# Kernel optimization log

Measured on AMD Instinct MI355X. Metric: run time of the kernel, lower is better.

Reference implementation:

```python
import jax, jax.numpy as jnp
import numpy as np


def setup_inputs() -> dict:
    key = jax.random.key(0)
    kq, kk, kv = jax.random.split(key, 3)
    B, H, S, D = 2, 16, 2048, 128
    q = jax.random.normal(kq, (B, H, S, D), dtype=jnp.float32)
    k = jax.random.normal(kk, (B, H, S, D), dtype=jnp.float32)
    v = jax.random.normal(kv, (B, H, S, D), dtype=jnp.float32)
    return {"q": q, "k": k, "v": v}


def reference(q, k, v):
    # qk: [B,H,S,S] full score matrix (faithful to the naive torch module)
    qk = jnp.einsum("bhsd,bhtd->bhst", q, k)
    m = jnp.max(qk, axis=-1, keepdims=True)          # row max
    p = jnp.exp(qk - m)                               # unnormalized probs
    # NOTE: original module computes lse but returns only the UNNORMALIZED o.
    o = jnp.einsum("bhst,bhtd->bhsd", p, v)
    return o
```

## Files before the change

### kernel.cpp

```cpp
#include <hip/hip_runtime.h>

typedef _Float16 f16x8  __attribute__((ext_vector_type(8)));
typedef _Float16 f16x4  __attribute__((ext_vector_type(4)));
typedef _Float16 f16x2  __attribute__((ext_vector_type(2)));
typedef float    f32x4  __attribute__((ext_vector_type(4)));
typedef float    f32x16 __attribute__((ext_vector_type(16)));

#define MFMA32(a, b, c) __builtin_amdgcn_mfma_f32_32x32x16_f16((a), (b), (c), 0, 0, 0)

static constexpr int SEQ   = 2048;
static constexpr int DIM   = 128;
static constexpr int QBLK  = 128;
static constexpr int KVBLK = 32;
static constexpr int NKT   = SEQ / KVBLK;
static constexpr int BH    = 2 * 16;
static constexpr int KSTR  = 136;
static constexpr int VSTR  = 40;

__global__ __launch_bounds__(256, 2)
void fa_fwd_kernel(const float* __restrict__ Qg, const float* __restrict__ Kg,
                   const float* __restrict__ Vg, float* __restrict__ Og)
{
    __shared__ __align__(16) _Float16 Ksh[KVBLK * KSTR];
    __shared__ __align__(16) _Float16 Vt[DIM * VSTR];

    const int tid  = threadIdx.x;
    const int wv   = tid >> 6;
    const int lane = tid & 63;
    const int lq   = lane & 31;
    const int lh   = lane >> 5;

    const int bi = blockIdx.x;
    const int bh = (bi & 7) + 8 * (bi >> 7);
    const int qt = (bi >> 3) & 15;

    const size_t base = (size_t)bh * SEQ * DIM;
    const float* Qp = Qg + base;
    const float* Kp = Kg + base;
    const float* Vp = Vg + base;
    float*       Op = Og + base;

    const int q0 = qt * QBLK + wv * 32;

    constexpr float LOG2E = 1.44269504088896340736f;
    f16x8 qh[8];
    {
        const float* qs = Qp + (size_t)(q0 + lq) * DIM + 8 * lh;
#pragma unroll
        for (int t = 0; t < 8; ++t) {
            const float4 a = *(const float4*)(qs + 16 * t);
            const float4 b = *(const float4*)(qs + 16 * t + 4);
            float xs[8] = {a.x, a.y, a.z, a.w, b.x, b.y, b.z, b.w};
            f16x8 h;
#pragma unroll
            for (int e = 0; e < 8; ++e) h[e] = (_Float16)(xs[e] * LOG2E);
            qh[t] = h;
        }
    }

    f32x16 acc[4];
#pragma unroll
    for (int a = 0; a < 4; ++a)
#pragma unroll
        for (int r = 0; r < 16; ++r) acc[a][r] = 0.0f;

    float mrow  = -3.0e38f;
    float mtrue = -3.0e38f;

    const int ksr = tid >> 3, kc0 = (tid & 7) * 16;
    const int vc  = tid & 31;
    const int vk  = (tid >> 5) * 4;
    const float* kb = Kp + (size_t)ksr * DIM + kc0;
    const float* vb = Vp + (size_t)vk * DIM + vc;

    float4 kreg[4];
    float  vreg[4][4];
#pragma unroll
    for (int t = 0; t < 4; ++t) kreg[t] = *(const float4*)(kb + t * 4);
#pragma unroll
    for (int j = 0; j < 4; ++j)
#pragma unroll
        for (int r = 0; r < 4; ++r) vreg[j][r] = vb[(size_t)r * DIM + 32 * j];

    for (int kt = 0; kt < NKT; ++kt) {
        __syncthreads();

#pragma unroll
        for (int g = 0; g < 2; ++g) {
            float xs[8] = {kreg[2*g].x, kreg[2*g].y, kreg[2*g].z, kreg[2*g].w,
                           kreg[2*g+1].x, kreg[2*g+1].y, kreg[2*g+1].z, kreg[2*g+1].w};
            f16x8 h;
#pragma unroll
            for (int e = 0; e < 8; ++e) h[e] = (_Float16)xs[e];
            *(f16x8*)((char*)Ksh + (ksr * KSTR + kc0 + 8 * g) * 2) = h;
        }
#pragma unroll
        for (int j = 0; j < 4; ++j) {
            const int d = vc + 32 * j;
            f16x4 tv = {(_Float16)vreg[j][0], (_Float16)vreg[j][1],
                        (_Float16)vreg[j][2], (_Float16)vreg[j][3]};
            *(f16x4*)((char*)Vt + (d * VSTR + vk) * 2) = tv;
        }
        __syncthreads();

        if (kt + 1 < NKT) {
            const float* ks_ = kb + (size_t)(kt + 1) * KVBLK * DIM;
            const float* vs_ = vb + (size_t)(kt + 1) * KVBLK * DIM;
#pragma unroll
            for (int t = 0; t < 4; ++t) kreg[t] = *(const float4*)(ks_ + t * 4);
#pragma unroll
            for (int j = 0; j < 4; ++j)
#pragma unroll
                for (int r = 0; r < 4; ++r) vreg[j][r] = vs_[(size_t)r * DIM + 32 * j];
        }

        f32x16 s0, s1;
#pragma unroll
        for (int r = 0; r < 16; ++r) { s0[r] = 0.0f; s1[r] = 0.0f; }
        __builtin_amdgcn_s_setprio(1);
#pragma unroll
        for (int t = 0; t < 4; ++t) {
            f16x8 ka = *(const f16x8*)((const char*)Ksh + (lq * KSTR + 32 * t + 8 * lh) * 2);
            f16x8 kc = *(const f16x8*)((const char*)Ksh + (lq * KSTR + 32 * t + 16 + 8 * lh) * 2);
            s0 = MFMA32(ka, qh[2 * t], s0);
            s1 = MFMA32(kc, qh[2 * t + 1], s1);
        }
        __builtin_amdgcn_s_setprio(0);
        f32x16 st = s0 + s1;

        float tmax = fmaxf(fmaxf(fmaxf(st[0], st[1]), fmaxf(st[2], st[3])),
                           fmaxf(fmaxf(st[4], st[5]), fmaxf(st[6], st[7])));
        tmax = fmaxf(tmax, fmaxf(fmaxf(fmaxf(st[8], st[9]), fmaxf(st[10], st[11])),
                                 fmaxf(fmaxf(st[12], st[13]), fmaxf(st[14], st[15]))));
        tmax = fmaxf(tmax, __shfl_xor(tmax, 32));
        mtrue = fmaxf(mtrue, tmax);

        if (!__all(tmax - mrow <= 6.0f)) {
            const float mn  = fmaxf(mrow, tmax);
            const float scl = __builtin_exp2f(mrow - mn);
            mrow = mn;
#pragma unroll
            for (int a = 0; a < 4; ++a)
#pragma unroll
                for (int r = 0; r < 16; ++r) acc[a][r] *= scl;
        }

        int pk[8];
#pragma unroll
        for (int i = 0; i < 8; ++i) {
            f16x2 e = {(_Float16)__builtin_exp2f(st[2 * i] - mrow),
                       (_Float16)__builtin_exp2f(st[2 * i + 1] - mrow)};
            pk[i] = __builtin_bit_cast(int, e);
        }

#pragma unroll
        for (int s = 0; s < 2; ++s) {
            const int z1 = __shfl_xor(lh ? pk[4*s+0] : pk[4*s+2], 32);
            const int z2 = __shfl_xor(lh ? pk[4*s+1] : pk[4*s+3], 32);
            union { int i[4]; f16x8 v; } u;
            u.i[0] = lh ? z1 : pk[4*s+0];
            u.i[1] = lh ? z2 : pk[4*s+1];
            u.i[2] = lh ? pk[4*s+2] : z1;
            u.i[3] = lh ? pk[4*s+3] : z2;
            const f16x8 pb = u.v;
            __builtin_amdgcn_s_setprio(1);
#pragma unroll
            for (int dm = 0; dm < 4; ++dm) {
                const int d = dm * 32 + lq;
                f16x8 va = *(const f16x8*)((const char*)Vt + (d * VSTR + 16 * s + 8 * lh) * 2);
                acc[dm] = MFMA32(va, pb, acc[dm]);
            }
            __builtin_amdgcn_s_setprio(0);
        }
    }

    const float fin = __builtin_exp2f(mrow - mtrue);
#pragma unroll
    for (int a = 0; a < 4; ++a)
#pragma unroll
        for (int r = 0; r < 16; ++r) acc[a][r] *= fin;

    float* ob = Op + (size_t)(q0 + lq) * DIM + 4 * lh;
#pragma unroll
    for (int dm = 0; dm < 4; ++dm)
#pragma unroll
        for (int kp = 0; kp < 4; ++kp) {
            f32x4 v4 = {acc[dm][4*kp], acc[dm][4*kp+1], acc[dm][4*kp+2], acc[dm][4*kp+3]};
            *(f32x4*)(ob + dm * 32 + kp * 8) = v4;
        }
}

extern "C" void kernel_launch(void* const* d_in, const int* in_sizes, int n_in,
                              void* d_out, int out_size, void* d_ws, size_t ws_size,
                              hipStream_t stream) {
    const float* q = (const float*)d_in[0];
    const float* k = (const float*)d_in[1];
    const float* v = (const float*)d_in[2];
    float* o = (float*)d_out;
    dim3 grid((SEQ / QBLK) * BH);
    fa_fwd_kernel<<<grid, dim3(256), 0, stream>>>(q, k, v, o);
}
```

Before: 121.5 us.

## Double KV tile to 64 rows and convert K/V to fp16 before the barrier

Doubles the KV tile from 32 to 64 keys, halving the number of loop iterations and their barriers. QK^T now computes two independent 32-key score tiles over the full head dimension instead of splitting the head dimension and summing. The fp16 conversion of prefetched K/V is moved ahead of the first barrier so only the LDS stores sit between the barriers, and the lazy-rescale threshold is loosened from 6 to 10. The cost is roughly double the prefetch registers (K/V staging plus fp16 copies) under a launch bound of 2 blocks per CU, which risks spills or lower occupancy, and the looser threshold lets fp16 probabilities grow larger.

```diff
diff --git a/kernel.cpp b/kernel.cpp
--- a/kernel.cpp
+++ b/kernel.cpp
@@ -11,11 +11,11 @@
 static constexpr int SEQ   = 2048;
 static constexpr int DIM   = 128;
 static constexpr int QBLK  = 128;
-static constexpr int KVBLK = 32;
+static constexpr int KVBLK = 64;
 static constexpr int NKT   = SEQ / KVBLK;
 static constexpr int BH    = 2 * 16;
 static constexpr int KSTR  = 136;
-static constexpr int VSTR  = 40;
+static constexpr int VSTR  = 72;
 
 __global__ __launch_bounds__(256, 2)
 void fa_fwd_kernel(const float* __restrict__ Qg, const float* __restrict__ Kg,
@@ -67,39 +67,49 @@
     float mrow  = -3.0e38f;
     float mtrue = -3.0e38f;
 
-    const int ksr = tid >> 3, kc0 = (tid & 7) * 16;
+    const int ksr = tid >> 2, kc0 = (tid & 3) * 32;
     const int vc  = tid & 31;
-    const int vk  = (tid >> 5) * 4;
+    const int vk  = (tid >> 5) * 8;
     const float* kb = Kp + (size_t)ksr * DIM + kc0;
     const float* vb = Vp + (size_t)vk * DIM + vc;
 
-    float4 kreg[4];
-    float  vreg[4][4];
-#pragma unroll
-    for (int t = 0; t < 4; ++t) kreg[t] = *(const float4*)(kb + t * 4);
+    float4 kreg[8];
+    float  vreg[4][8];
+#pragma unroll
+    for (int t = 0; t < 8; ++t) kreg[t] = *(const float4*)(kb + t * 4);
 #pragma unroll
     for (int j = 0; j < 4; ++j)
 #pragma unroll
-        for (int r = 0; r < 4; ++r) vreg[j][r] = vb[(size_t)r * DIM + 32 * j];
+        for (int r = 0; r < 8; ++r) vreg[j][r] = vb[(size_t)r * DIM + 32 * j];
 
     for (int kt = 0; kt < NKT; ++kt) {
-        __syncthreads();
-
-#pragma unroll
-        for (int g = 0; g < 2; ++g) {
+        f16x8 kh16[4], vh16[4];
+#pragma unroll
+        for (int g = 0; g < 4; ++g) {
             float xs[8] = {kreg[2*g].x, kreg[2*g].y, kreg[2*g].z, kreg[2*g].w,
                            kreg[2*g+1].x, kreg[2*g+1].y, kreg[2*g+1].z, kreg[2*g+1].w};
             f16x8 h;
 #pragma unroll
             for (int e = 0; e < 8; ++e) h[e] = (_Float16)xs[e];
-            *(f16x8*)((char*)Ksh + (ksr * KSTR + kc0 + 8 * g) * 2) = h;
-        }
+            kh16[g] = h;
+        }
+#pragma unroll
+        for (int j = 0; j < 4; ++j) {
+            f16x8 h;
+#pragma unroll
+            for (int r = 0; r < 8; ++r) h[r] = (_Float16)vreg[j][r];
+            vh16[j] = h;
+        }
+
+        __syncthreads();
+
+#pragma unroll
+        for (int g = 0; g < 4; ++g)
+            *(f16x8*)((char*)Ksh + (ksr * KSTR + kc0 + 8 * g) * 2) = kh16[g];
 #pragma unroll
         for (int j = 0; j < 4; ++j) {
             const int d = vc + 32 * j;
-            f16x4 tv = {(_Float16)vreg[j][0], (_Float16)vreg[j][1],
-                        (_Float16)vreg[j][2], (_Float16)vreg[j][3]};
-            *(f16x4*)((char*)Vt + (d * VSTR + vk) * 2) = tv;
+            *(f16x8*)((char*)Vt + (d * VSTR + vk) * 2) = vh16[j];
         }
         __syncthreads();
 
@@ -107,11 +117,11 @@
             const float* ks_ = kb + (size_t)(kt + 1) * KVBLK * DIM;
             const float* vs_ = vb + (size_t)(kt + 1) * KVBLK * DIM;
 #pragma unroll
-            for (int t = 0; t < 4; ++t) kreg[t] = *(const float4*)(ks_ + t * 4);
+            for (int t = 0; t < 8; ++t) kreg[t] = *(const float4*)(ks_ + t * 4);
 #pragma unroll
             for (int j = 0; j < 4; ++j)
 #pragma unroll
-                for (int r = 0; r < 4; ++r) vreg[j][r] = vs_[(size_t)r * DIM + 32 * j];
+                for (int r = 0; r < 8; ++r) vreg[j][r] = vs_[(size_t)r * DIM + 32 * j];
         }
 
         f32x16 s0, s1;
@@ -119,23 +129,21 @@
         for (int r = 0; r < 16; ++r) { s0[r] = 0.0f; s1[r] = 0.0f; }
         __builtin_amdgcn_s_setprio(1);
 #pragma unroll
-        for (int t = 0; t < 4; ++t) {
-            f16x8 ka = *(const f16x8*)((const char*)Ksh + (lq * KSTR + 32 * t + 8 * lh) * 2);
-            f16x8 kc = *(const f16x8*)((const char*)Ksh + (lq * KSTR + 32 * t + 16 + 8 * lh) * 2);
-            s0 = MFMA32(ka, qh[2 * t], s0);
-            s1 = MFMA32(kc, qh[2 * t + 1], s1);
+        for (int t = 0; t < 8; ++t) {
+            f16x8 ka = *(const f16x8*)((const char*)Ksh + (lq * KSTR + 16 * t + 8 * lh) * 2);
+            f16x8 kc = *(const f16x8*)((const char*)Ksh + ((lq + 32) * KSTR + 16 * t + 8 * lh) * 2);
+            s0 = MFMA32(ka, qh[t], s0);
+            s1 = MFMA32(kc, qh[t], s1);
         }
         __builtin_amdgcn_s_setprio(0);
-        f32x16 st = s0 + s1;
-
-        float tmax = fmaxf(fmaxf(fmaxf(st[0], st[1]), fmaxf(st[2], st[3])),
-                           fmaxf(fmaxf(st[4], st[5]), fmaxf(st[6], st[7])));
-        tmax = fmaxf(tmax, fmaxf(fmaxf(fmaxf(st[8], st[9]), fmaxf(st[10], st[11])),
-                                 fmaxf(fmaxf(st[12], st[13]), fmaxf(st[14], st[15]))));
+
+        float tmax = fmaxf(s0[0], s1[0]);
+#pragma unroll
+        for (int r = 1; r < 16; ++r) tmax = fmaxf(tmax, fmaxf(s0[r], s1[r]));
         tmax = fmaxf(tmax, __shfl_xor(tmax, 32));
         mtrue = fmaxf(mtrue, tmax);
 
-        if (!__all(tmax - mrow <= 6.0f)) {
+        if (!__all(tmax - mrow <= 10.0f)) {
             const float mn  = fmaxf(mrow, tmax);
             const float scl = __builtin_exp2f(mrow - mn);
             mrow = mn;
@@ -145,23 +153,28 @@
                 for (int r = 0; r < 16; ++r) acc[a][r] *= scl;
         }
 
-        int pk[8];
+        int pk[16];
 #pragma unroll
         for (int i = 0; i < 8; ++i) {
-            f16x2 e = {(_Float16)__builtin_exp2f(st[2 * i] - mrow),
-                       (_Float16)__builtin_exp2f(st[2 * i + 1] - mrow)};
-            pk[i] = __builtin_bit_cast(int, e);
-        }
-
-#pragma unroll
-        for (int s = 0; s < 2; ++s) {
-            const int z1 = __shfl_xor(lh ? pk[4*s+0] : pk[4*s+2], 32);
-            const int z2 = __shfl_xor(lh ? pk[4*s+1] : pk[4*s+3], 32);
+            f16x2 e0 = {(_Float16)__builtin_exp2f(s0[2*i] - mrow),
+                        (_Float16)__builtin_exp2f(s0[2*i+1] - mrow)};
+            f16x2 e1 = {(_Float16)__builtin_exp2f(s1[2*i] - mrow),
+                        (_Float16)__builtin_exp2f(s1[2*i+1] - mrow)};
+            pk[i]     = __builtin_bit_cast(int, e0);
+            pk[8 + i] = __builtin_bit_cast(int, e1);
+        }
+
+#pragma unroll
+        for (int s = 0; s < 4; ++s) {
+            const int b  = (s >> 1) * 8;
+            const int sl = s & 1;
+            const int z1 = __shfl_xor(lh ? pk[b+4*sl+0] : pk[b+4*sl+2], 32);
+            const int z2 = __shfl_xor(lh ? pk[b+4*sl+1] : pk[b+4*sl+3], 32);
             union { int i[4]; f16x8 v; } u;
-            u.i[0] = lh ? z1 : pk[4*s+0];
-            u.i[1] = lh ? z2 : pk[4*s+1];
-            u.i[2] = lh ? pk[4*s+2] : z1;
-            u.i[3] = lh ? pk[4*s+3] : z2;
+            u.i[0] = lh ? z1 : pk[b+4*sl+0];
+            u.i[1] = lh ? z2 : pk[b+4*sl+1];
+            u.i[2] = lh ? pk[b+4*sl+2] : z1;
+            u.i[3] = lh ? pk[b+4*sl+3] : z2;
             const f16x8 pb = u.v;
             __builtin_amdgcn_s_setprio(1);
 #pragma unroll
```

After: 129.0 us. 1.06x slower.

## Double-buffer K/V LDS tiles to remove one barrier per iteration

Applied to the files above, without the earlier changes.

Splits the K and transposed V shared-memory tiles into two buffers. The next tile is staged into the alternate buffer while the current one is consumed, so each KV iteration needs a single __syncthreads instead of two. Global loads are issued two tiles ahead. This doubles LDS usage and adds a scheduling barrier, which may constrain compiler interleaving of the stores with the MFMA work.

```diff
diff --git a/kernel.cpp b/kernel.cpp
--- a/kernel.cpp
+++ b/kernel.cpp
@@ -21,8 +21,8 @@
 void fa_fwd_kernel(const float* __restrict__ Qg, const float* __restrict__ Kg,
                    const float* __restrict__ Vg, float* __restrict__ Og)
 {
-    __shared__ __align__(16) _Float16 Ksh[KVBLK * KSTR];
-    __shared__ __align__(16) _Float16 Vt[DIM * VSTR];
+    __shared__ __align__(16) _Float16 Ksh[2][KVBLK * KSTR];
+    __shared__ __align__(16) _Float16 Vt[2][DIM * VSTR];
 
     const int tid  = threadIdx.x;
     const int wv   = tid >> 6;
@@ -75,16 +75,8 @@
 
     float4 kreg[4];
     float  vreg[4][4];
-#pragma unroll
-    for (int t = 0; t < 4; ++t) kreg[t] = *(const float4*)(kb + t * 4);
-#pragma unroll
-    for (int j = 0; j < 4; ++j)
-#pragma unroll
-        for (int r = 0; r < 4; ++r) vreg[j][r] = vb[(size_t)r * DIM + 32 * j];
-
-    for (int kt = 0; kt < NKT; ++kt) {
-        __syncthreads();
-
+
+    auto stage = [&](int b) {
 #pragma unroll
         for (int g = 0; g < 2; ++g) {
             float xs[8] = {kreg[2*g].x, kreg[2*g].y, kreg[2*g].z, kreg[2*g].w,
@@ -92,36 +84,49 @@
             f16x8 h;
 #pragma unroll
             for (int e = 0; e < 8; ++e) h[e] = (_Float16)xs[e];
-            *(f16x8*)((char*)Ksh + (ksr * KSTR + kc0 + 8 * g) * 2) = h;
+            *(f16x8*)((char*)&Ksh[b][0] + (ksr * KSTR + kc0 + 8 * g) * 2) = h;
         }
 #pragma unroll
         for (int j = 0; j < 4; ++j) {
             const int d = vc + 32 * j;
             f16x4 tv = {(_Float16)vreg[j][0], (_Float16)vreg[j][1],
                         (_Float16)vreg[j][2], (_Float16)vreg[j][3]};
-            *(f16x4*)((char*)Vt + (d * VSTR + vk) * 2) = tv;
-        }
+            *(f16x4*)((char*)&Vt[b][0] + (d * VSTR + vk) * 2) = tv;
+        }
+    };
+    auto loadT = [&](int t) {
+        const float* ks_ = kb + (size_t)t * KVBLK * DIM;
+        const float* vs_ = vb + (size_t)t * KVBLK * DIM;
+#pragma unroll
+        for (int u = 0; u < 4; ++u) kreg[u] = *(const float4*)(ks_ + u * 4);
+#pragma unroll
+        for (int j = 0; j < 4; ++j)
+#pragma unroll
+            for (int r = 0; r < 4; ++r) vreg[j][r] = vs_[(size_t)r * DIM + 32 * j];
+    };
+
+    loadT(0);
+    stage(0);
+    loadT(1);
+
+    for (int kt = 0; kt < NKT; ++kt) {
+        const int cur = kt & 1;
         __syncthreads();
 
-        if (kt + 1 < NKT) {
-            const float* ks_ = kb + (size_t)(kt + 1) * KVBLK * DIM;
-            const float* vs_ = vb + (size_t)(kt + 1) * KVBLK * DIM;
-#pragma unroll
-            for (int t = 0; t < 4; ++t) kreg[t] = *(const float4*)(ks_ + t * 4);
-#pragma unroll
-            for (int j = 0; j < 4; ++j)
-#pragma unroll
-                for (int r = 0; r < 4; ++r) vreg[j][r] = vs_[(size_t)r * DIM + 32 * j];
-        }
-
+        if (kt + 1 < NKT) stage(cur ^ 1);
+        if (kt + 2 < NKT) loadT(kt + 2);
+        __builtin_amdgcn_sched_barrier(0);
+
+        const char* Kc = (const char*)&Ksh[cur][0];
+        const char* Vc = (const char*)&Vt[cur][0];
         f32x16 s0, s1;
 #pragma unroll
         for (int r = 0; r < 16; ++r) { s0[r] = 0.0f; s1[r] = 0.0f; }
         __builtin_amdgcn_s_setprio(1);
 #pragma unroll
         for (int t = 0; t < 4; ++t) {
-            f16x8 ka = *(const f16x8*)((const char*)Ksh + (lq * KSTR + 32 * t + 8 * lh) * 2);
-            f16x8 kc = *(const f16x8*)((const char*)Ksh + (lq * KSTR + 32 * t + 16 + 8 * lh) * 2);
+            f16x8 ka = *(const f16x8*)(Kc + (lq * KSTR + 32 * t + 8 * lh) * 2);
+            f16x8 kc = *(const f16x8*)(Kc + (lq * KSTR + 32 * t + 16 + 8 * lh) * 2);
             s0 = MFMA32(ka, qh[2 * t], s0);
             s1 = MFMA32(kc, qh[2 * t + 1], s1);
         }
@@ -167,7 +172,7 @@
 #pragma unroll
             for (int dm = 0; dm < 4; ++dm) {
                 const int d = dm * 32 + lq;
-                f16x8 va = *(const f16x8*)((const char*)Vt + (d * VSTR + 16 * s + 8 * lh) * 2);
+                f16x8 va = *(const f16x8*)(Vc + (d * VSTR + 16 * s + 8 * lh) * 2);
                 acc[dm] = MFMA32(va, pb, acc[dm]);
             }
             __builtin_amdgcn_s_setprio(0);
```

New measurement: 117.0 us. -3.7%, faster.
